# Kernel tuning notes

Hardware: AMD Instinct MI355X
Metric: run time of the kernel (lower is better)

The kernel has to match this reference:

```python
import jax, jax.numpy as jnp
import numpy as np

B, S, D, H, DH = 2, 2048, 1024, 16, 64
R_ATTN, R_OUT, I, R_FC1, R_FC2 = 32, 512, 4096, 512, 512
LN_EPS = 1e-5


def _layernorm(x, g, b):
    mu = jnp.mean(x, axis=-1, keepdims=True)
    var = jnp.mean(jnp.square(x - mu), axis=-1, keepdims=True)
    return (x - mu) * jax.lax.rsqrt(var + LN_EPS) * g + b


def setup_inputs() -> dict:
    key = jax.random.key(0)
    ks = jax.random.split(key, 16)
    std = 0.02
    return {
        'hidden_states': jax.random.normal(ks[0], (B, S, D), jnp.float32),
        'ln1_g': jnp.ones((D,), jnp.float32),
        'ln1_b': jnp.zeros((D,), jnp.float32),
        'ln2_g': jnp.ones((D,), jnp.float32),
        'ln2_b': jnp.zeros((D,), jnp.float32),
        'q_U': jax.random.normal(ks[1], (D, H, R_ATTN), jnp.float32) * std,
        'q_V': jax.random.normal(ks[2], (H, R_ATTN, DH), jnp.float32) * std,
        'q_b': jnp.zeros((H, DH), jnp.float32),
        'k_U': jax.random.normal(ks[3], (D, H, R_ATTN), jnp.float32) * std,
        'k_V': jax.random.normal(ks[4], (H, R_ATTN, DH), jnp.float32) * std,
        'k_b': jnp.zeros((H, DH), jnp.float32),
        'v_U': jax.random.normal(ks[5], (D, H, R_ATTN), jnp.float32) * std,
        'v_V': jax.random.normal(ks[6], (H, R_ATTN, DH), jnp.float32) * std,
        'v_b': jnp.zeros((H, DH), jnp.float32),
        'out_U': jax.random.normal(ks[7], (D, R_OUT), jnp.float32) * std,
        'out_V': jax.random.normal(ks[8], (R_OUT, D), jnp.float32) * std,
        'out_b': jnp.zeros((D,), jnp.float32),
        'fc1_U': jax.random.normal(ks[9], (D, R_FC1), jnp.float32) * std,
        'fc1_V': jax.random.normal(ks[10], (R_FC1, I), jnp.float32) * std,
        'fc1_b': jnp.zeros((I,), jnp.float32),
        'fc2_U': jax.random.normal(ks[11], (I, R_FC2), jnp.float32) * std,
        'fc2_V': jax.random.normal(ks[12], (R_FC2, D), jnp.float32) * std,
        'fc2_b': jnp.zeros((D,), jnp.float32),
    }


def reference(hidden_states, ln1_g, ln1_b, ln2_g, ln2_b,
              q_U, q_V, q_b, k_U, k_V, k_b, v_U, v_V, v_b,
              out_U, out_V, out_b, fc1_U, fc1_V, fc1_b, fc2_U, fc2_V, fc2_b):
    Bx, Sx, Dx = hidden_states.shape
    scale = 1.0 / np.sqrt(DH).astype(np.float32)
    x = _layernorm(hidden_states, ln1_g, ln1_b)
    # low-rank per-head QKV: [B,S,D]x[D,H,r]x[H,r,dh] -> [B,H,S,dh]
    Q = jnp.einsum('bsd,dhr,hre->bhse', x, q_U, q_V) + q_b[None, :, None, :]
    K = jnp.einsum('bsd,dhr,hre->bhse', x, k_U, k_V) + k_b[None, :, None, :]
    V = jnp.einsum('bsd,dhr,hre->bhse', x, v_U, v_V) + v_b[None, :, None, :]
    scores = jnp.einsum('bhse,bhte->bhst', Q, K) * scale  # [B,H,S,S]
    causal = jnp.tril(jnp.ones((Sx, Sx), bool))
    neg_inf = jnp.finfo(scores.dtype).min
    scores = jnp.where(causal, scores, neg_inf)
    probs = jax.nn.softmax(scores, axis=-1)
    Y = jnp.einsum('bhst,bhte->bhse', probs, V)
    Y = Y.transpose(0, 2, 1, 3).reshape(Bx, Sx, Dx)  # merge heads
    Y = (Y @ out_U) @ out_V + out_b
    h = hidden_states + Y
    z = _layernorm(h, ln2_g, ln2_b)
    h1 = jax.nn.gelu((z @ fc1_U) @ fc1_V + fc1_b, approximate=False)
    h2 = (h1 @ fc2_U) @ fc2_V + fc2_b
    return h + h2
```

## Files before the change

### kernel.cpp

```cpp
#include <hip/hip_runtime.h>
#include <cstdint>
#include <cstddef>


#define NTOK 4096
#define DM   1024
#define SEQ  2048

typedef __attribute__((ext_vector_type(8))) __bf16 bf16x8;
typedef __attribute__((ext_vector_type(4))) __bf16 bf16x4;
typedef __attribute__((ext_vector_type(4))) float  f32x4;

__device__ __forceinline__ f32x4 mfma16(bf16x8 a, bf16x8 b, f32x4 c) {
  return __builtin_amdgcn_mfma_f32_16x16x32_bf16(a, b, c, 0, 0, 0);
}

__device__ __forceinline__ void gload16(const __bf16* g, __bf16* l) {
  __builtin_amdgcn_global_load_lds(
      (const __attribute__((address_space(1))) void*)g,
      (__attribute__((address_space(3))) void*)l, 16, 0, 0);
}

__device__ __forceinline__ void xcd_map(int flat, int gx, int gy,
                                        int BM, int BN, int& bm, int& bn) {
  int nwg = gx * gy;
  if ((nwg & 7) == 0) {
    int cpx = nwg >> 3;
    int xcd = flat & 7;
    int loc = flat >> 3;
    int w = cpx >> 4;
    if ((gy & 15) == 0 && (cpx & 15) == 0 && w > 0 && gx % w == 0) {
      int rcols = gx / w;
      bm = ((xcd / rcols) * 16 + loc / w) * BM;
      bn = ((xcd % rcols) * w + loc % w) * BN;
      return;
    }
    flat = xcd * cpx + loc;
  }
  bm = (flat / gx) * BM;
  bn = (flat % gx) * BN;
}

__global__ __launch_bounds__(256) void transpose_k(const float* __restrict__ in,
                                                   __bf16* __restrict__ out,
                                                   int R, int C) {
  __shared__ __bf16 t[32][33];
  int tx = threadIdx.x & 31, ty = threadIdx.x >> 5;
  int r0 = blockIdx.y * 32, c0 = blockIdx.x * 32;
#pragma unroll
  for (int i = 0; i < 32; i += 8)
    t[ty + i][tx] = (__bf16)in[(size_t)(r0 + ty + i) * C + c0 + tx];
  __syncthreads();
#pragma unroll
  for (int i = 0; i < 32; i += 8)
    out[(size_t)(c0 + ty + i) * R + r0 + tx] = t[tx][ty + i];
}

__global__ __launch_bounds__(256) void prep_k(
    const float* __restrict__ qb, const float* __restrict__ kb,
    const float* __restrict__ vb, float* __restrict__ bqkv,
    const float* __restrict__ outU, __bf16* __restrict__ outUT,
    const float* __restrict__ outV, __bf16* __restrict__ outVT,
    const float* __restrict__ f1U,  __bf16* __restrict__ f1UT,
    const float* __restrict__ f1V,  __bf16* __restrict__ f1VT,
    const float* __restrict__ f2V,  __bf16* __restrict__ f2VT,
    const float* __restrict__ f2U,  __bf16* __restrict__ f2UT,
    __bf16* __restrict__ outUc) {
  int blk = blockIdx.x;
  if (blk < 12) {
    int i = blk * 256 + threadIdx.x;
    bqkv[i] = (i < 1024) ? qb[i] : (i < 2048 ? kb[i - 1024] : vb[i - 2048]);
    return;
  }
  int t = blk - 12;
  if (t >= 6144) {
    int i = (t - 6144) * 2048 + threadIdx.x * 8;
    float4 a = *(const float4*)(outU + i);
    float4 b = *(const float4*)(outU + i + 4);
    bf16x8 o = {(__bf16)a.x, (__bf16)a.y, (__bf16)a.z, (__bf16)a.w,
                (__bf16)b.x, (__bf16)b.y, (__bf16)b.z, (__bf16)b.w};
    *(bf16x8*)(outUc + i) = o;
    return;
  }
  const float* in; __bf16* out; int R, C;
  if (t < 512)       { in = outU; out = outUT; R = 1024; C = 512;  }
  else if (t < 1024) { in = outV; out = outVT; R = 512;  C = 1024; t -= 512; }
  else if (t < 1536) { in = f1U;  out = f1UT;  R = 1024; C = 512;  t -= 1024; }
  else if (t < 3584) { in = f1V;  out = f1VT;  R = 512;  C = 4096; t -= 1536; }
  else if (t < 4096) { in = f2V;  out = f2VT;  R = 512;  C = 1024; t -= 3584; }
  else               { in = f2U;  out = f2UT;  R = 4096; C = 512;  t -= 4096; }
  int ct = C >> 5;
  int c0 = (t % ct) * 32, r0 = (t / ct) * 32;
  __shared__ __bf16 tt[32][33];
  int tx = threadIdx.x & 31, ty = threadIdx.x >> 5;
#pragma unroll
  for (int i = 0; i < 32; i += 8)
    tt[ty + i][tx] = (__bf16)in[(size_t)(r0 + ty + i) * C + c0 + tx];
  __syncthreads();
#pragma unroll
  for (int i = 0; i < 32; i += 8)
    out[(size_t)(c0 + ty + i) * R + r0 + tx] = tt[tx][ty + i];
}

__global__ __launch_bounds__(256) void trans_v(const __bf16* __restrict__ qkv,
                                               __bf16* __restrict__ VT) {
  __shared__ __bf16 t[32][33];
  int tx = threadIdx.x & 31, ty = threadIdx.x >> 5;
  int bh = blockIdx.z, b = bh >> 4, h = bh & 15;
  int k0 = blockIdx.x * 32, d0 = blockIdx.y * 32;
#pragma unroll
  for (int i = 0; i < 32; i += 8)
    t[ty + i][tx] = qkv[(size_t)(b * SEQ + k0 + ty + i) * 3072 + 2048 + h * 64 + d0 + tx];
  __syncthreads();
#pragma unroll
  for (int i = 0; i < 32; i += 8)
    VT[(size_t)(bh * 64 + d0 + ty + i) * SEQ + k0 + tx] = t[tx][ty + i];
}

__global__ __launch_bounds__(256) void combine_uv(const float* __restrict__ qU,
                                                  const float* __restrict__ qV,
                                                  const float* __restrict__ kU,
                                                  const float* __restrict__ kV,
                                                  const float* __restrict__ vU,
                                                  const float* __restrict__ vV,
                                                  __bf16* __restrict__ WT) {
  __shared__ float sV[2048];
  int tid = threadIdx.x;
  int blk = blockIdx.x;
  int sel = blk >> 7;
  int rem = blk & 127;
  int h = rem >> 3, dc = rem & 7;
  int d0 = dc << 7;
  const float* U = sel == 0 ? qU : (sel == 1 ? kU : vU);
  const float* V = sel == 0 ? qV : (sel == 1 ? kV : vV);
  for (int i = tid; i < 2048; i += 256) sV[i] = V[h * 2048 + i];
  int d = d0 + (tid & 127);
  int eh = tid >> 7;
  const float* up = U + (size_t)d * 512 + h * 32;
  float u[32];
#pragma unroll
  for (int i = 0; i < 8; i++)
    *(float4*)&u[i * 4] = *(const float4*)(up + i * 4);
  __syncthreads();
  int e0 = eh * 32;
#pragma unroll
  for (int eg = 0; eg < 8; eg++) {
    float ax = 0.f, ay = 0.f, az = 0.f, aw = 0.f;
#pragma unroll
    for (int r = 0; r < 32; r++) {
      float4 v4 = *(const float4*)&sV[r * 64 + e0 + eg * 4];
      ax += u[r] * v4.x; ay += u[r] * v4.y;
      az += u[r] * v4.z; aw += u[r] * v4.w;
    }
    size_t prow = (size_t)(sel * 1024 + h * 64 + e0 + eg * 4) * 1024 + d;
    WT[prow]        = (__bf16)ax;
    WT[prow + 1024] = (__bf16)ay;
    WT[prow + 2048] = (__bf16)az;
    WT[prow + 3072] = (__bf16)aw;
  }
}

__global__ __launch_bounds__(256) void cast_k(const float* __restrict__ in,
                                              __bf16* __restrict__ out, int n) {
  int i = blockIdx.x * 256 + threadIdx.x;
  if (i < n) out[i] = (__bf16)in[i];
}

__global__ __launch_bounds__(256) void merge4_k(const float* __restrict__ p,
                                                __bf16* __restrict__ out) {
  int i = blockIdx.x * 256 + threadIdx.x;
  float s = (p[i] + p[i + 2097152]) + (p[i + 4194304] + p[i + 6291456]);
  out[i] = (__bf16)s;
}

template <int TWO>
__global__ __launch_bounds__(256) void ln_k(const float* __restrict__ x,
                                            const __bf16* __restrict__ x2,
                                            const float* __restrict__ g,
                                            const float* __restrict__ b,
                                            __bf16* __restrict__ out) {
  int row = blockIdx.x, tid = threadIdx.x;
  const float* xr = x + (size_t)row * DM;
  float v[4], s = 0.f, ss = 0.f;
#pragma unroll
  for (int i = 0; i < 4; i++) {
    int c = i * 256 + tid;
    v[i] = xr[c];
    if (TWO) v[i] += (float)x2[(size_t)row * DM + c];
    s += v[i]; ss += v[i] * v[i];
  }
#pragma unroll
  for (int m = 1; m < 64; m <<= 1) { s += __shfl_xor(s, m); ss += __shfl_xor(ss, m); }
  __shared__ float rs_[4], rss[4];
  if ((tid & 63) == 0) { rs_[tid >> 6] = s; rss[tid >> 6] = ss; }
  __syncthreads();
  s  = rs_[0] + rs_[1] + rs_[2] + rs_[3];
  ss = rss[0] + rss[1] + rss[2] + rss[3];
  float mu  = s * (1.f / 1024.f);
  float var = ss * (1.f / 1024.f) - mu * mu;
  float rstd = rsqrtf(var + 1e-5f);
#pragma unroll
  for (int i = 0; i < 4; i++) {
    int c = i * 256 + tid;
    out[(size_t)row * DM + c] = (__bf16)((v[i] - mu) * rstd * g[c] + b[c]);
  }
}

template <int EPI, int BN>
__global__ __launch_bounds__(256) void gemm_bt(const __bf16* __restrict__ A,
                                               const __bf16* __restrict__ BT,
                                               void* __restrict__ Cv,
                                               const float* __restrict__ bias,
                                               const float* __restrict__ resF,
                                               const __bf16* __restrict__ resB,
                                               int M, int N, int K) {
  constexpr int WR = (BN == 128) ? 4 : 2;
  __shared__ alignas(16) __bf16 la[2][128 * 32];
  __shared__ alignas(16) __bf16 lb[2][BN * 32];
  int tid = threadIdx.x;
  int lane = tid & 63;
  int wave = tid >> 6;
  int quad = lane >> 4, l15 = lane & 15;
  int flat = blockIdx.y * gridDim.x + blockIdx.x;
  int bm, bn;
  xcd_map(flat, gridDim.x, gridDim.y, 128, BN, bm, bn);
  int wm = (BN == 128) ? (wave >> 1) * 64 : wave * 32;
  int wn = (BN == 128) ? (wave & 1) * 64 : 0;
  int lr = lane >> 2;
  int lc = (((lane & 3) ^ ((lr >> 1) & 3))) * 8;
  const __bf16* ga = A  + (size_t)(bm + wave * 32 + lr) * K + lc;
  const __bf16* gb = BT + (size_t)(bn + wave * (BN == 128 ? 32 : 16) + lr) * K + lc;
  int ksw = ((l15 >> 1) & 3) * 8;
  f32x4 acc[WR][4] = {};

  auto stage = [&](int k0, int b) {
    __bf16* lab = &la[b][wave * 1024];
    gload16(ga + k0, lab);
    gload16(ga + (size_t)16 * K + k0, lab + 512);
    if (BN == 128) {
      __bf16* lbb = &lb[b][wave * 1024];
      gload16(gb + k0, lbb);
      gload16(gb + (size_t)16 * K + k0, lbb + 512);
    } else {
      gload16(gb + k0, &lb[b][wave * 512]);
    }
  };

  stage(0, 0);
  __syncthreads();
  for (int k0 = 0; k0 < K; k0 += 32) {
    int b = (k0 >> 5) & 1;
    if (k0 + 32 < K) stage(k0 + 32, b ^ 1);
    bf16x8 af[WR], bfr[4];
#pragma unroll
    for (int i = 0; i < WR; i++)
      af[i] = *(const bf16x8*)&la[b][(wm + i * 16 + l15) * 32 + (quad * 8 ^ ksw)];
#pragma unroll
    for (int j = 0; j < 4; j++)
      bfr[j] = *(const bf16x8*)&lb[b][(wn + j * 16 + l15) * 32 + (quad * 8 ^ ksw)];
#pragma unroll
    for (int i = 0; i < WR; i++)
#pragma unroll
      for (int j = 0; j < 4; j++)
        acc[i][j] = mfma16(af[i], bfr[j], acc[i][j]);
    __syncthreads();
  }
#pragma unroll
  for (int i = 0; i < WR; i++) {
#pragma unroll
    for (int j = 0; j < 4; j++) {
      int col = bn + wn + j * 16 + l15;
      float bv = bias ? bias[col] : 0.f;
#pragma unroll
      for (int r = 0; r < 4; r++) {
        int row = bm + wm + i * 16 + quad * 4 + r;
        size_t idx = (size_t)row * N + col;
        float v = acc[i][j][r] + bv;
        if (EPI == 0) {
          ((__bf16*)Cv)[idx] = (__bf16)v;
        } else if (EPI == 1) {
          float y = 0.79788456080286536f * fmaf(0.044715f * v, v * v, v);
          float u = exp2f(y * 2.885390081777926f);
          float th = (u - 1.f) / (u + 1.f);
          v = 0.5f * v * (1.f + th);
          ((__bf16*)Cv)[idx] = (__bf16)v;
        } else {
          v += resF[idx] + (float)resB[idx];
          ((float*)Cv)[idx] = v;
        }
      }
    }
  }
}

__global__ __launch_bounds__(256) void gemm_bt64s(const __bf16* __restrict__ A,
                                                  const __bf16* __restrict__ BT,
                                                  __bf16* __restrict__ C,
                                                  int M, int N, int K) {
  __shared__ alignas(16) __bf16 la[2][64 * 32];
  __shared__ alignas(16) __bf16 lb[2][64 * 32];
  int tid = threadIdx.x;
  int lane = tid & 63;
  int wave = tid >> 6;
  int quad = lane >> 4, l15 = lane & 15;
  int flat = blockIdx.y * gridDim.x + blockIdx.x;
  int bm, bn;
  xcd_map(flat, gridDim.x, gridDim.y, 64, 64, bm, bn);
  int lr = tid >> 2;
  int lc = (((tid & 3) ^ ((lr >> 1) & 3))) * 8;
  const __bf16* ga = A  + (size_t)(bm + lr) * K + lc;
  const __bf16* gb = BT + (size_t)(bn + lr) * K + lc;
  int ksw = ((l15 >> 1) & 3) * 8;
  f32x4 acc[4] = {};

  auto stage = [&](int k0, int b) {
    gload16(ga + k0, &la[b][tid * 8]);
    gload16(gb + k0, &lb[b][tid * 8]);
  };

  stage(0, 0);
  __syncthreads();
  for (int k0 = 0; k0 < K; k0 += 32) {
    int b = (k0 >> 5) & 1;
    if (k0 + 32 < K) stage(k0 + 32, b ^ 1);
    bf16x8 af = *(const bf16x8*)&la[b][(wave * 16 + l15) * 32 + (quad * 8 ^ ksw)];
    bf16x8 bfr[4];
#pragma unroll
    for (int j = 0; j < 4; j++)
      bfr[j] = *(const bf16x8*)&lb[b][(j * 16 + l15) * 32 + (quad * 8 ^ ksw)];
#pragma unroll
    for (int j = 0; j < 4; j++)
      acc[j] = mfma16(af, bfr[j], acc[j]);
    __syncthreads();
  }
#pragma unroll
  for (int j = 0; j < 4; j++) {
    int col = bn + j * 16 + l15;
#pragma unroll
    for (int r = 0; r < 4; r++) {
      int row = bm + wave * 16 + quad * 4 + r;
      C[(size_t)row * N + col] = (__bf16)acc[j][r];
    }
  }
}

template <int ATOMIC>
__global__ __launch_bounds__(256) void gemm_sk(const __bf16* __restrict__ A,
                                               const __bf16* __restrict__ BT,
                                               float* __restrict__ Cf,
                                               int M, int N, int K, int KS) {
  __shared__ alignas(16) __bf16 la[2][128 * 32];
  __shared__ alignas(16) __bf16 lb[2][128 * 32];
  int tid = threadIdx.x;
  int lane = tid & 63;
  int wave = tid >> 6;
  int quad = lane >> 4, l15 = lane & 15;
  int flat = blockIdx.y * gridDim.x + blockIdx.x;
  int bm, bn;
  xcd_map(flat, gridDim.x, gridDim.y, 128, 128, bm, bn);
  int wm = (wave >> 1) * 64, wn = (wave & 1) * 64;
  int klen = K / KS;
  int kbeg = blockIdx.z * klen, kend = kbeg + klen;
  int lr = lane >> 2;
  int lc = (((lane & 3) ^ ((lr >> 1) & 3))) * 8;
  const __bf16* ga = A  + (size_t)(bm + wave * 32 + lr) * K + lc;
  const __bf16* gb = BT + (size_t)(bn + wave * 32 + lr) * K + lc;
  int ksw = ((l15 >> 1) & 3) * 8;
  f32x4 acc[4][4] = {};

  auto stage = [&](int k0, int b) {
    __bf16* lab = &la[b][wave * 1024];
    __bf16* lbb = &lb[b][wave * 1024];
    gload16(ga + k0, lab);
    gload16(ga + (size_t)16 * K + k0, lab + 512);
    gload16(gb + k0, lbb);
    gload16(gb + (size_t)16 * K + k0, lbb + 512);
  };

  stage(kbeg, 0);
  __syncthreads();
  for (int k0 = kbeg; k0 < kend; k0 += 32) {
    int b = ((k0 - kbeg) >> 5) & 1;
    if (k0 + 32 < kend) stage(k0 + 32, b ^ 1);
    bf16x8 af[4], bfr[4];
#pragma unroll
    for (int i = 0; i < 4; i++)
      af[i] = *(const bf16x8*)&la[b][(wm + i * 16 + l15) * 32 + (quad * 8 ^ ksw)];
#pragma unroll
    for (int j = 0; j < 4; j++)
      bfr[j] = *(const bf16x8*)&lb[b][(wn + j * 16 + l15) * 32 + (quad * 8 ^ ksw)];
#pragma unroll
    for (int i = 0; i < 4; i++)
#pragma unroll
      for (int j = 0; j < 4; j++)
        acc[i][j] = mfma16(af[i], bfr[j], acc[i][j]);
    __syncthreads();
  }
  float* out = ATOMIC ? Cf : Cf + (size_t)blockIdx.z * M * N;
#pragma unroll
  for (int i = 0; i < 4; i++)
#pragma unroll
    for (int j = 0; j < 4; j++) {
      int col = bn + wn + j * 16 + l15;
#pragma unroll
      for (int r = 0; r < 4; r++) {
        int row = bm + wm + i * 16 + quad * 4 + r;
        if (ATOMIC) atomicAdd(&out[(size_t)row * N + col], acc[i][j][r]);
        else        out[(size_t)row * N + col] = acc[i][j][r];
      }
    }
}

#define JOB(q, a, b) ((uint32_t)(q) | ((uint32_t)(a) << 8) | ((uint32_t)(b) << 16))
__device__ const uint32_t JOBTAB[24] = {
  JOB(7, 0, 16),  JOB(15, 0, 16), JOB(15, 16, 32),
  JOB(14, 0, 15), JOB(14, 15, 30),
  JOB(6, 0, 14),  JOB(13, 0, 14), JOB(13, 14, 28),
  JOB(12, 0, 13), JOB(12, 13, 26),
  JOB(5, 0, 12),  JOB(11, 0, 12), JOB(11, 12, 24),
  JOB(10, 0, 11), JOB(10, 11, 22),
  JOB(4, 0, 10),  JOB(9, 0, 10),  JOB(9, 10, 20),
  JOB(8, 0, 9),   JOB(8, 9, 18),
  JOB(3, 0, 8),   JOB(2, 0, 6),   JOB(1, 0, 4),   JOB(0, 0, 2),
};

__global__ __launch_bounds__(512, 6) void attn_k(const __bf16* __restrict__ QKV,
                                                 const __bf16* __restrict__ VT,
                                                 __bf16* __restrict__ Y,
                                                 float* __restrict__ Opart,
                                                 float* __restrict__ lpart) {
  const float SC = 0.18033688011112042f;
  const float C2 = 23.083120654223414f;
  __shared__ alignas(16) __bf16 lk[2][64 * 64];
  __shared__ alignas(16) __bf16 lv[2][64 * 64];
  __shared__ alignas(16) __bf16 P[8][16 * 72];
  int tid = threadIdx.x;
  int wave = tid >> 6, lane = tid & 63;
  int quad = lane >> 4, l15 = lane & 15;
  int bh = blockIdx.x & 31;
  int job = blockIdx.x >> 5;
  uint32_t jt = JOBTAB[job];
  int qb = jt & 255, kbeg = (jt >> 8) & 255, kend = (jt >> 16) & 255;
  bool split = qb >= 8;
  int b = bh >> 4, h = bh & 15;
  int q0w = (qb << 7) + wave * 16;
  const size_t RS = 3 * DM;
  const __bf16* base = QKV + (size_t)b * SEQ * RS;
  const __bf16* vtb  = VT + (size_t)bh * 64 * SEQ;

  const __bf16* qp = base + (size_t)(q0w + l15) * RS + h * 64 + quad * 8;
  bf16x8 aq0 = *(const bf16x8*)qp;
  bf16x8 aq1 = *(const bf16x8*)(qp + 32);

  int srow = tid >> 3, schunk = tid & 7;
  int sswz = (schunk ^ (srow & 7)) << 3;
  const __bf16* gk_src = base + (size_t)srow * RS + DM + h * 64 + sswz;
  const __bf16* gv_src = vtb + (size_t)srow * SEQ + sswz;

  int c0 = (quad ^ (l15 & 7)) << 3;
  int c1 = ((quad + 4) ^ (l15 & 7)) << 3;

  f32x4 zero4 = {0.f, 0.f, 0.f, 0.f};
  f32x4 O[4] = {zero4, zero4, zero4, zero4};
  float l_i = 0.f;

  int ntiles = kend - kbeg;

  gload16(gk_src + ((size_t)kbeg << 6) * RS, &lk[0][tid * 8]);
  gload16(gv_src + ((size_t)kbeg << 6),      &lv[0][tid * 8]);
  __syncthreads();

  for (int t = 0; t < ntiles; t++) {
    int kt = kbeg + t;
    int cur = t & 1;
    if (t + 1 < ntiles) {
      size_t kn = (size_t)(kt + 1) << 6;
      gload16(gk_src + kn * RS, &lk[cur ^ 1][tid * 8]);
      gload16(gv_src + kn,      &lv[cur ^ 1][tid * 8]);
    }
    int k0 = kt << 6;
    if (k0 <= q0w + 15) {
      f32x4 s[4] = {zero4, zero4, zero4, zero4};
#pragma unroll
      for (int gk = 0; gk < 4; gk++) {
        const __bf16* kr = &lk[cur][(gk * 16 + l15) * 64];
        bf16x8 kb0 = *(const bf16x8*)(kr + c0);
        bf16x8 kb1 = *(const bf16x8*)(kr + c1);
        s[gk] = mfma16(kb0, aq0, s[gk]);
        s[gk] = mfma16(kb1, aq1, s[gk]);
      }
      if (k0 + 63 <= q0w) {
#pragma unroll
        for (int gk = 0; gk < 4; gk++) {
          float p0 = exp2f(fmaf(s[gk][0], SC, -C2));
          float p1 = exp2f(fmaf(s[gk][1], SC, -C2));
          float p2 = exp2f(fmaf(s[gk][2], SC, -C2));
          float p3 = exp2f(fmaf(s[gk][3], SC, -C2));
          l_i += (p0 + p1) + (p2 + p3);
          bf16x4 pw = {(__bf16)p0, (__bf16)p1, (__bf16)p2, (__bf16)p3};
          *(bf16x4*)&P[wave][l15 * 72 + gk * 16 + quad * 4] = pw;
        }
      } else {
        int qrow = q0w + l15;
#pragma unroll
        for (int gk = 0; gk < 4; gk++) {
          int kb = k0 + gk * 16 + quad * 4;
          float p0 = (kb     <= qrow) ? exp2f(fmaf(s[gk][0], SC, -C2)) : 0.f;
          float p1 = (kb + 1 <= qrow) ? exp2f(fmaf(s[gk][1], SC, -C2)) : 0.f;
          float p2 = (kb + 2 <= qrow) ? exp2f(fmaf(s[gk][2], SC, -C2)) : 0.f;
          float p3 = (kb + 3 <= qrow) ? exp2f(fmaf(s[gk][3], SC, -C2)) : 0.f;
          l_i += (p0 + p1) + (p2 + p3);
          bf16x4 pw = {(__bf16)p0, (__bf16)p1, (__bf16)p2, (__bf16)p3};
          *(bf16x4*)&P[wave][l15 * 72 + gk * 16 + quad * 4] = pw;
        }
      }
      bf16x8 ap0 = *(const bf16x8*)&P[wave][l15 * 72 + quad * 8];
      bf16x8 ap1 = *(const bf16x8*)&P[wave][l15 * 72 + 32 + quad * 8];
#pragma unroll
      for (int nt = 0; nt < 4; nt++) {
        const __bf16* vr = &lv[cur][(nt * 16 + l15) * 64];
        bf16x8 bv0 = *(const bf16x8*)(vr + c0);
        bf16x8 bv1 = *(const bf16x8*)(vr + c1);
        O[nt] = mfma16(ap0, bv0, O[nt]);
        O[nt] = mfma16(ap1, bv1, O[nt]);
      }
    }
    __syncthreads();
  }

  l_i += __shfl_xor(l_i, 16);
  l_i += __shfl_xor(l_i, 32);
  if (!split) {
#pragma unroll
    for (int r = 0; r < 4; r++) {
      float inv = 1.f / __shfl(l_i, quad * 4 + r);
      size_t orow = (size_t)(b * SEQ + q0w + quad * 4 + r);
      __bf16* yp = Y + orow * DM + h * 64 + l15;
      yp[0]  = (__bf16)(O[0][r] * inv);
      yp[16] = (__bf16)(O[1][r] * inv);
      yp[32] = (__bf16)(O[2][r] * inv);
      yp[48] = (__bf16)(O[3][r] * inv);
    }
  } else {
#pragma unroll
    for (int r = 0; r < 4; r++) {
      int row = (q0w - 1024) + quad * 4 + r;
      float* op = Opart + (((size_t)bh << 10) + row) * 64 + l15;
      atomicAdd(op +  0, O[0][r]);
      atomicAdd(op + 16, O[1][r]);
      atomicAdd(op + 32, O[2][r]);
      atomicAdd(op + 48, O[3][r]);
    }
    if (quad == 0)
      atomicAdd(&lpart[((size_t)bh << 10) + (q0w - 1024) + l15], l_i);
  }
}

__global__ __launch_bounds__(256) void norm_k(const float* __restrict__ Op,
                                              const float* __restrict__ lp,
                                              __bf16* __restrict__ Y) {
  int idx = blockIdx.x * 256 + threadIdx.x;
  int dh = idx & 63;
  int row = (idx >> 6) & 1023;
  int bh = idx >> 16;
  int b = bh >> 4, h = bh & 15;
  float inv = 1.f / lp[(bh << 10) + row];
  Y[(size_t)(b * SEQ + 1024 + row) * DM + h * 64 + dh] = (__bf16)(Op[idx] * inv);
}

extern "C" void kernel_launch(void* const* d_in, const int* in_sizes, int n_in,
                              void* d_out, int out_size, void* d_ws, size_t ws_size,
                              hipStream_t stream) {
  (void)in_sizes; (void)n_in; (void)out_size;
  const float* hidden = (const float*)d_in[0];
  const float* ln1_g  = (const float*)d_in[1];
  const float* ln1_b  = (const float*)d_in[2];
  const float* ln2_g  = (const float*)d_in[3];
  const float* ln2_b  = (const float*)d_in[4];
  const float* q_U = (const float*)d_in[5];
  const float* q_V = (const float*)d_in[6];
  const float* q_b = (const float*)d_in[7];
  const float* k_U = (const float*)d_in[8];
  const float* k_V = (const float*)d_in[9];
  const float* k_b = (const float*)d_in[10];
  const float* v_U = (const float*)d_in[11];
  const float* v_V = (const float*)d_in[12];
  const float* v_b = (const float*)d_in[13];
  const float* out_U = (const float*)d_in[14];
  const float* out_V = (const float*)d_in[15];
  const float* out_b = (const float*)d_in[16];
  const float* fc1_U = (const float*)d_in[17];
  const float* fc1_V = (const float*)d_in[18];
  const float* fc1_b = (const float*)d_in[19];
  const float* fc2_U = (const float*)d_in[20];
  const float* fc2_V = (const float*)d_in[21];
  const float* fc2_b = (const float*)d_in[22];

  const size_t MB = 1u << 20;
  char* ws = (char*)d_ws;
  bool big = ws_size >= 128 * MB;
  __bf16* outUT = (__bf16*)(ws + 0 * MB);
  __bf16* outVT = (__bf16*)(ws + 1 * MB);
  __bf16* f1UT  = (__bf16*)(ws + 2 * MB);
  __bf16* f1VT  = (__bf16*)(ws + 3 * MB);
  __bf16* f2VT  = (__bf16*)(ws + 7 * MB);
  float*  bqkv  = (float*) (ws + 8 * MB);
  __bf16* wqkvT = (__bf16*)(ws + 9 * MB);
  __bf16* f2UT  = big ? (__bf16*)(ws + 55 * MB)
                      : (__bf16*)(ws + 9 * MB);
  __bf16* xln   = (__bf16*)(ws + 15 * MB);
  __bf16* yattn = (__bf16*)(ws + 15 * MB);
  __bf16* zbuf  = (__bf16*)(ws + 15 * MB);
  float*  t3f32 = (float*) (ws + 15 * MB);
  __bf16* t3bf  = (__bf16*)(ws + 19 * MB);
  __bf16* qkv   = (__bf16*)(ws + 23 * MB);
  __bf16* h1c   = big ? (__bf16*)(ws + 64 * MB)
                      : (__bf16*)(ws + 23 * MB);
  float*  t3p   = (float*) (ws + 96 * MB);
  __bf16* tbuf  = (__bf16*)(ws + 43 * MB);
  __bf16* VT    = (__bf16*)(ws + 47 * MB);
  __bf16* hres  = (__bf16*)(ws + 47 * MB);
  __bf16* WoutT = (__bf16*)(ws + 59 * MB);
  __bf16* outUc = (__bf16*)(ws + 61 * MB);
  float* Opart = (float*)d_out;
  float* lpart = (float*)d_out + 2097152;

  prep_k<<<big ? 6412 : 4108, 256, 0, stream>>>(
      q_b, k_b, v_b, bqkv, out_U, outUT, out_V, outVT,
      fc1_U, f1UT, fc1_V, f1VT, fc2_V, f2VT, fc2_U, f2UT, outUc);
  combine_uv<<<384, 256, 0, stream>>>(q_U, q_V, k_U, k_V, v_U, v_V, wqkvT);
  if (big)
    gemm_bt<0, 64><<<dim3(16, 8), 256, 0, stream>>>(outVT, outUc, WoutT,
                                                    nullptr, nullptr, nullptr,
                                                    1024, 1024, 512);

  ln_k<0><<<NTOK, 256, 0, stream>>>(hidden, nullptr, ln1_g, ln1_b, xln);
  gemm_bt<0, 128><<<dim3(24, 32), 256, 0, stream>>>(xln, wqkvT, qkv, bqkv,
                                                    nullptr, nullptr, NTOK, 3072, 1024);
  if (!big)
    transpose_k<<<dim3(16, 128), 256, 0, stream>>>(fc2_U, f2UT, 4096, 512);
  trans_v<<<dim3(64, 2, 32), 256, 0, stream>>>(qkv, VT);
  hipMemsetAsync(d_out, 0, (size_t)8519680, stream);
  attn_k<<<768, 512, 0, stream>>>(qkv, VT, yattn, Opart, lpart);
  norm_k<<<8192, 256, 0, stream>>>(Opart, lpart, yattn);
  if (big) {
    gemm_bt<0, 64><<<dim3(16, 32), 256, 0, stream>>>(yattn, WoutT, hres, out_b,
                                                     nullptr, nullptr, NTOK, 1024, 1024);
  } else {
    gemm_bt64s<<<dim3(8, 64), 256, 0, stream>>>(yattn, outUT, tbuf, NTOK, 512, 1024);
    gemm_bt<0, 64><<<dim3(16, 32), 256, 0, stream>>>(tbuf, outVT, hres, out_b,
                                                     nullptr, nullptr, NTOK, 1024, 512);
  }
  ln_k<1><<<NTOK, 256, 0, stream>>>(hidden, hres, ln2_g, ln2_b, zbuf);
  gemm_bt64s<<<dim3(8, 64), 256, 0, stream>>>(zbuf, f1UT, tbuf, NTOK, 512, 1024);
  if (big) {
    gemm_bt<1, 128><<<dim3(32, 32), 256, 0, stream>>>(tbuf, f1VT, h1c, fc1_b,
                                                      nullptr, nullptr, NTOK, 4096, 512);
    gemm_sk<0><<<dim3(4, 32, 4), 256, 0, stream>>>(h1c, f2UT, t3p,
                                                   NTOK, 512, 4096, 4);
    merge4_k<<<8192, 256, 0, stream>>>(t3p, t3bf);
  } else {
    for (int mc = 0; mc < 2; mc++) {
      __bf16* tchunk = tbuf + (size_t)mc * 2048 * 512;
      gemm_bt<1, 128><<<dim3(32, 16), 256, 0, stream>>>(tchunk, f1VT, h1c, fc1_b,
                                                        nullptr, nullptr, 2048, 4096, 512);
      hipMemsetAsync(t3f32, 0, (size_t)2048 * 512 * 4, stream);
      gemm_sk<1><<<dim3(4, 16, 4), 256, 0, stream>>>(h1c, f2UT, t3f32,
                                                     2048, 512, 4096, 4);
      cast_k<<<4096, 256, 0, stream>>>(t3f32, t3bf + (size_t)mc * 2048 * 512,
                                       2048 * 512);
    }
  }
  gemm_bt<3, 64><<<dim3(16, 32), 256, 0, stream>>>(t3bf, f2VT, (float*)d_out, fc2_b,
                                                   hidden, hres, NTOK, 1024, 512);
}
```

Before: 376.5 us.

## Triple-buffer GEMM LDS staging with partial vmcnt waits instead of full syncs

Converts the three GEMM kernels from double to triple buffering of LDS tiles, prefetching two k-steps ahead. Each full __syncthreads is replaced by an explicit s_waitcnt vmcnt(N) that waits only for the older stage, followed by a raw barrier, so one stage of global loads stays in flight across iterations. This is meant to hide global-to-LDS latency better. In exchange it uses 1.5x the LDS, which may lower occupancy, and its correctness depends on the hand-counted outstanding loads per stage.

```diff
diff --git a/kernel.cpp b/kernel.cpp
--- a/kernel.cpp
+++ b/kernel.cpp
@@ -19,6 +19,13 @@
   __builtin_amdgcn_global_load_lds(
       (const __attribute__((address_space(1))) void*)g,
       (__attribute__((address_space(3))) void*)l, 16, 0, 0);
+}
+
+template <int N> __device__ __forceinline__ void waitcnt_vm() {
+  if constexpr (N == 0)      asm volatile("s_waitcnt vmcnt(0)" ::: "memory");
+  else if constexpr (N == 2) asm volatile("s_waitcnt vmcnt(2)" ::: "memory");
+  else if constexpr (N == 3) asm volatile("s_waitcnt vmcnt(3)" ::: "memory");
+  else                       asm volatile("s_waitcnt vmcnt(4)" ::: "memory");
 }
 
 __device__ __forceinline__ void xcd_map(int flat, int gx, int gy,
@@ -214,9 +221,10 @@
                                                const float* __restrict__ resF,
                                                const __bf16* __restrict__ resB,
                                                int M, int N, int K) {
-  constexpr int WR = (BN == 128) ? 4 : 2;
-  __shared__ alignas(16) __bf16 la[2][128 * 32];
-  __shared__ alignas(16) __bf16 lb[2][BN * 32];
+  constexpr int WR  = (BN == 128) ? 4 : 2;
+  constexpr int NLD = (BN == 128) ? 4 : 3;
+  __shared__ alignas(16) __bf16 la[3][128 * 32];
+  __shared__ alignas(16) __bf16 lb[3][BN * 32];
   int tid = threadIdx.x;
   int lane = tid & 63;
   int wave = tid >> 6;
@@ -247,10 +255,13 @@
   };
 
   stage(0, 0);
-  __syncthreads();
+  stage(32, 1);
+  waitcnt_vm<NLD>();
+  __builtin_amdgcn_s_barrier();
   for (int k0 = 0; k0 < K; k0 += 32) {
-    int b = (k0 >> 5) & 1;
-    if (k0 + 32 < K) stage(k0 + 32, b ^ 1);
+    int b = (k0 >> 5) % 3;
+    bool pf = (k0 + 64 < K);
+    if (pf) stage(k0 + 64, (b + 2) % 3);
     bf16x8 af[WR], bfr[4];
 #pragma unroll
     for (int i = 0; i < WR; i++)
@@ -263,7 +274,10 @@
 #pragma unroll
       for (int j = 0; j < 4; j++)
         acc[i][j] = mfma16(af[i], bfr[j], acc[i][j]);
-    __syncthreads();
+    if (k0 + 32 < K) {
+      if (pf) waitcnt_vm<NLD>(); else waitcnt_vm<0>();
+      __builtin_amdgcn_s_barrier();
+    }
   }
 #pragma unroll
   for (int i = 0; i < WR; i++) {
@@ -297,8 +311,8 @@
                                                   const __bf16* __restrict__ BT,
                                                   __bf16* __restrict__ C,
                                                   int M, int N, int K) {
-  __shared__ alignas(16) __bf16 la[2][64 * 32];
-  __shared__ alignas(16) __bf16 lb[2][64 * 32];
+  __shared__ alignas(16) __bf16 la[3][64 * 32];
+  __shared__ alignas(16) __bf16 lb[3][64 * 32];
   int tid = threadIdx.x;
   int lane = tid & 63;
   int wave = tid >> 6;
@@ -319,10 +333,13 @@
   };
 
   stage(0, 0);
-  __syncthreads();
+  stage(32, 1);
+  waitcnt_vm<2>();
+  __builtin_amdgcn_s_barrier();
   for (int k0 = 0; k0 < K; k0 += 32) {
-    int b = (k0 >> 5) & 1;
-    if (k0 + 32 < K) stage(k0 + 32, b ^ 1);
+    int b = (k0 >> 5) % 3;
+    bool pf = (k0 + 64 < K);
+    if (pf) stage(k0 + 64, (b + 2) % 3);
     bf16x8 af = *(const bf16x8*)&la[b][(wave * 16 + l15) * 32 + (quad * 8 ^ ksw)];
     bf16x8 bfr[4];
 #pragma unroll
@@ -331,7 +348,10 @@
 #pragma unroll
     for (int j = 0; j < 4; j++)
       acc[j] = mfma16(af, bfr[j], acc[j]);
-    __syncthreads();
+    if (k0 + 32 < K) {
+      if (pf) waitcnt_vm<2>(); else waitcnt_vm<0>();
+      __builtin_amdgcn_s_barrier();
+    }
   }
 #pragma unroll
   for (int j = 0; j < 4; j++) {
@@ -349,8 +369,8 @@
                                                const __bf16* __restrict__ BT,
                                                float* __restrict__ Cf,
                                                int M, int N, int K, int KS) {
-  __shared__ alignas(16) __bf16 la[2][128 * 32];
-  __shared__ alignas(16) __bf16 lb[2][128 * 32];
+  __shared__ alignas(16) __bf16 la[3][128 * 32];
+  __shared__ alignas(16) __bf16 lb[3][128 * 32];
   int tid = threadIdx.x;
   int lane = tid & 63;
   int wave = tid >> 6;
@@ -378,10 +398,13 @@
   };
 
   stage(kbeg, 0);
-  __syncthreads();
+  stage(kbeg + 32, 1);
+  waitcnt_vm<4>();
+  __builtin_amdgcn_s_barrier();
   for (int k0 = kbeg; k0 < kend; k0 += 32) {
-    int b = ((k0 - kbeg) >> 5) & 1;
-    if (k0 + 32 < kend) stage(k0 + 32, b ^ 1);
+    int b = ((k0 - kbeg) >> 5) % 3;
+    bool pf = (k0 + 64 < kend);
+    if (pf) stage(k0 + 64, (b + 2) % 3);
     bf16x8 af[4], bfr[4];
 #pragma unroll
     for (int i = 0; i < 4; i++)
@@ -394,7 +417,10 @@
 #pragma unroll
       for (int j = 0; j < 4; j++)
         acc[i][j] = mfma16(af[i], bfr[j], acc[i][j]);
-    __syncthreads();
+    if (k0 + 32 < kend) {
+      if (pf) waitcnt_vm<4>(); else waitcnt_vm<0>();
+      __builtin_amdgcn_s_barrier();
+    }
   }
   float* out = ATOMIC ? Cf : Cf + (size_t)blockIdx.z * M * N;
 #pragma unroll
```

New measurement: 437.2 us. 16.1% more time.
